# Optimization experiments

Measured on AMD Instinct MI355X. Metric: run time of the kernel, lower is better.

Reference implementation:

```python
import jax, jax.numpy as jnp
import numpy as np

B, IMG, P, C_IN, D, NH, DEPTH, E, TOPK, NCLS = 8, 224, 16, 3, 768, 12, 12, 8, 2, 1000
DH = 4 * D
HD = D // NH
GRID = IMG // P
NPAT = GRID * GRID
MOE_POS = (1, 3, 5, 7, 9, 11)
N_DENSE = DEPTH - len(MOE_POS)
N_MOE = len(MOE_POS)


def setup_inputs() -> dict:
    key = jax.random.key(0)
    ks = iter(jax.random.split(key, 32))
    n = lambda shape: jax.random.normal(next(ks), shape, jnp.float32) * 0.02
    return dict(
        x=jax.random.normal(next(ks), (B, C_IN, IMG, IMG), jnp.float32),
        patch_w=n((D, C_IN * P * P)), patch_b=jnp.zeros((D,), jnp.float32),
        cls_token=n((1, 1, D)), pos_embed=n((1, NPAT + 1, D)),
        ln1_w=jnp.ones((DEPTH, D), jnp.float32), ln1_b=jnp.zeros((DEPTH, D), jnp.float32),
        qkv_w=n((DEPTH, 3 * D, D)), qkv_b=jnp.zeros((DEPTH, 3 * D), jnp.float32),
        proj_w=n((DEPTH, D, D)), proj_b=jnp.zeros((DEPTH, D), jnp.float32),
        ln2_w=jnp.ones((DEPTH, D), jnp.float32), ln2_b=jnp.zeros((DEPTH, D), jnp.float32),
        fc1_w=n((N_DENSE, DH, D)), fc1_b=jnp.zeros((N_DENSE, DH), jnp.float32),
        fc2_w=n((N_DENSE, D, DH)), fc2_b=jnp.zeros((N_DENSE, D), jnp.float32),
        gate_w=n((N_MOE, E, D)), gate_b=jnp.zeros((N_MOE, E), jnp.float32),
        exp_w1=n((N_MOE, E, DH, D)), exp_b1=jnp.zeros((N_MOE, E, DH), jnp.float32),
        exp_w2=n((N_MOE, E, D, DH)), exp_b2=jnp.zeros((N_MOE, E, D), jnp.float32),
        norm_w=jnp.ones((D,), jnp.float32), norm_b=jnp.zeros((D,), jnp.float32),
        head_w=n((NCLS, D)), head_b=jnp.zeros((NCLS,), jnp.float32),
    )


def _ln(x, w, b):
    m = x.mean(-1, keepdims=True)
    v = ((x - m) ** 2).mean(-1, keepdims=True)
    return (x - m) / jnp.sqrt(v + 1e-5) * w + b


def _attn(x, qw, qb, pw, pb):
    Bn, N, _ = x.shape
    qkv = (x @ qw.T + qb).reshape(Bn, N, 3, NH, HD).transpose(2, 0, 3, 1, 4)
    q, k, v = qkv[0], qkv[1], qkv[2]  # [B, NH, N, HD]
    a = jax.nn.softmax(jnp.einsum('bhnd,bhmd->bhnm', q, k) * HD ** -0.5, -1)
    o = jnp.einsum('bhnm,bhmd->bhnd', a, v).transpose(0, 2, 1, 3).reshape(Bn, N, D)
    return o @ pw.T + pb


def _moe(x, gw, gb, w1, b1, w2, b2):
    # FMoETransformerMLP with NaiveGate: top-2 routing, softmax over top-k logits.
    shp = x.shape
    xf = x.reshape(-1, D)  # [T, D]
    logits = xf @ gw.T + gb  # [T, E]
    vals, idx = jax.lax.top_k(logits, TOPK)
    sc = jax.nn.softmax(vals, -1)  # [T, TOPK]
    comb = (jax.nn.one_hot(idx, E, dtype=xf.dtype) * sc[..., None]).sum(1)  # [T, E]
    h = jax.nn.gelu(jnp.einsum('td,ehd->teh', xf, w1) + b1, approximate=False)
    y = jnp.einsum('teh,edh->ted', h, w2) + b2
    return (y * comb[..., None]).sum(1).reshape(shp)


def reference(x, patch_w, patch_b, cls_token, pos_embed, ln1_w, ln1_b, qkv_w, qkv_b, proj_w, proj_b, ln2_w, ln2_b, fc1_w, fc1_b, fc2_w, fc2_b, gate_w, gate_b, exp_w1, exp_b1, exp_w2, exp_b2, norm_w, norm_b, head_w, head_b):
    patches = x.reshape(B, C_IN, GRID, P, GRID, P).transpose(0, 2, 4, 1, 3, 5).reshape(B, NPAT, C_IN * P * P)
    z = jnp.concatenate([jnp.broadcast_to(cls_token, (B, 1, D)), patches @ patch_w.T + patch_b], 1) + pos_embed
    di = mi = 0
    for i in range(DEPTH):
        z = z + _attn(_ln(z, ln1_w[i], ln1_b[i]), qkv_w[i], qkv_b[i], proj_w[i], proj_b[i])
        h2 = _ln(z, ln2_w[i], ln2_b[i])
        if i in MOE_POS:
            z = z + _moe(h2, gate_w[mi], gate_b[mi], exp_w1[mi], exp_b1[mi], exp_w2[mi], exp_b2[mi])
            mi += 1
        else:
            z = z + (jax.nn.gelu(h2 @ fc1_w[di].T + fc1_b[di], approximate=False) @ fc2_w[di].T + fc2_b[di])
            di += 1
    z = _ln(z, norm_w, norm_b)
    return z[:, 0] @ head_w.T + head_b
```

## Files before the change

kernel.cpp:

```cpp
#include <hip/hip_runtime.h>
#include <hip/hip_bf16.h>
#include <math.h>

#define B_     8
#define IMG_   224
#define PATCH_ 16
#define CIN_   3
#define D_     768
#define NH_    12
#define DEPTH_ 12
#define NE_    8
#define NCLS_  1000
#define DH_    3072
#define HD_    64
#define GRD_   14
#define NPAT_  196
#define NTOK_  197
#define T_     (B_*NTOK_)
#define TP_    (B_*NPAT_)
#define NSLOT_ (T_*2)

typedef __bf16 bf16_t;
typedef __bf16 bf16x8 __attribute__((ext_vector_type(8)));
typedef __bf16 bf16x4 __attribute__((ext_vector_type(4)));
typedef float  f32x4  __attribute__((ext_vector_type(4)));

static __device__ __forceinline__ float gelu_f(float x){
    return 0.5f * x * (1.0f + erff(x * 0.70710678118654752440f));
}

__global__ __launch_bounds__(256) void k_cvt(const float* __restrict__ in,
                                             bf16_t* __restrict__ out, int n){
    int i = (blockIdx.x*256 + threadIdx.x)*8;
    if (i >= n) return;
    float4 a = *reinterpret_cast<const float4*>(in + i);
    float4 b = *reinterpret_cast<const float4*>(in + i + 4);
    bf16x8 h;
    h[0]=(bf16_t)a.x; h[1]=(bf16_t)a.y; h[2]=(bf16_t)a.z; h[3]=(bf16_t)a.w;
    h[4]=(bf16_t)b.x; h[5]=(bf16_t)b.y; h[6]=(bf16_t)b.z; h[7]=(bf16_t)b.w;
    *reinterpret_cast<bf16x8*>(out + i) = h;
}

__global__ void k_patch_gather(const float* __restrict__ x, bf16_t* __restrict__ pbuf){
    int idx = blockIdx.x*256 + threadIdx.x;
    if (idx >= TP_*D_) return;
    int k  = idx % D_;
    int tp = idx / D_;
    int p  = tp % NPAT_, b = tp / NPAT_;
    int c  = k >> 8;
    int ij = k & 255;
    int i  = ij >> 4, j = ij & 15;
    int gi = p / GRD_, gj = p % GRD_;
    pbuf[idx] = (bf16_t)x[(((size_t)b*CIN_ + c)*IMG_ + gi*PATCH_ + i)*IMG_ + gj*PATCH_ + j];
}

template<int ACT, int GATHER, int MOE, int OUTBF, int KSPLIT, int PARTIAL, int BMT, int NW>
__global__ __launch_bounds__(NW*64) void k_mgemm(
    const bf16_t* __restrict__ A, const int* __restrict__ gidx,
    const bf16_t* __restrict__ W, const float* __restrict__ bias,
    void* __restrict__ Cout, int M, int N, int K,
    const int* __restrict__ moff, const int* __restrict__ mcnt)
{
    __shared__ __align__(16) bf16_t As[BMT*64];
    __shared__ __align__(16) bf16_t Bs[128*64];
    const int tid = threadIdx.x, lane = tid & 63, w = tid >> 6;
    int row_begin, Mhi, ksid;
    if (MOE) {
        const int e = blockIdx.z;
        const int o = moff[e], c = mcnt[e];
        const int rb = (KSPLIT == 2) ? (int)(blockIdx.y >> 1) : (int)blockIdx.y;
        ksid = (KSPLIT == 2) ? (int)(blockIdx.y & 1) : 0;
        row_begin = o + rb*BMT;
        Mhi = o + c;
        if (row_begin >= Mhi) return;
        W += (size_t)e*N*K;
        if (!PARTIAL) bias += (size_t)e*N;
    } else {
        row_begin = blockIdx.y*BMT;
        ksid = (KSPLIT == 2) ? (int)blockIdx.z : 0;
        Mhi = M;
    }
    const int bn = blockIdx.x*128;
    const int KL = K / KSPLIT;

    const bf16_t* aG[2];
    int aOff[2];
    #pragma unroll
    for (int i = 0; i < 2; ++i) {
        const int s = w*2 + i;
        const int row_l = s*8 + (lane >> 3);
        const int cc = (lane & 7) ^ (row_l & 7);
        const int gg = min(row_begin + row_l, Mhi - 1);
        const int tok = GATHER ? (gidx[gg] >> 1) : gg;
        aG[i] = A + (size_t)tok*K + ksid*KL + cc*8;
        aOff[i] = s*512;
    }
    constexpr int NB = 16/NW;
    const bf16_t* wG[NB];
    int wOff[NB];
    #pragma unroll
    for (int j = 0; j < NB; ++j) {
        const int s = w*NB + j;
        const int row_l = s*8 + (lane >> 3);
        const int cc = (lane & 7) ^ (row_l & 7);
        wG[j] = W + (size_t)(bn + row_l)*K + ksid*KL + cc*8;
        wOff[j] = s*512;
    }
    const int wm = (w >> 1)*32, wn = (w & 1)*64;
    const int fr = lane & 15, kg = lane >> 4;
    int offA[2][2], offB[2][4];
    #pragma unroll
    for (int ks = 0; ks < 2; ++ks) {
        #pragma unroll
        for (int t = 0; t < 2; ++t) {
            const int ra = wm + t*16 + fr;
            offA[ks][t] = ra*128 + (((ks*4 + kg) ^ (ra & 7)) << 4);
        }
        #pragma unroll
        for (int t = 0; t < 4; ++t) {
            const int rb2 = wn + t*16 + fr;
            offB[ks][t] = rb2*128 + (((ks*4 + kg) ^ (rb2 & 7)) << 4);
        }
    }

    f32x4 acc[2][4] = {};
    const int nt = KL >> 6;
    for (int t = 0; t < nt; ++t) {
        if (t) __syncthreads();
        #pragma unroll
        for (int i = 0; i < 2; ++i) {
            __builtin_amdgcn_global_load_lds(
                (const __attribute__((address_space(1))) void*)(aG[i]),
                (__attribute__((address_space(3))) void*)(&As[aOff[i]]), 16, 0, 0);
            aG[i] += 64;
        }
        #pragma unroll
        for (int j = 0; j < NB; ++j) {
            __builtin_amdgcn_global_load_lds(
                (const __attribute__((address_space(1))) void*)(wG[j]),
                (__attribute__((address_space(3))) void*)(&Bs[wOff[j]]), 16, 0, 0);
            wG[j] += 64;
        }
        __syncthreads();
        const char* baseA = (const char*)&As[0];
        const char* baseB = (const char*)&Bs[0];
        #pragma unroll
        for (int ks = 0; ks < 2; ++ks) {
            bf16x8 af[2], bf[4];
            #pragma unroll
            for (int t2 = 0; t2 < 2; ++t2)
                af[t2] = *reinterpret_cast<const bf16x8*>(baseA + offA[ks][t2]);
            #pragma unroll
            for (int t2 = 0; t2 < 4; ++t2)
                bf[t2] = *reinterpret_cast<const bf16x8*>(baseB + offB[ks][t2]);
            #pragma unroll
            for (int mt = 0; mt < 2; ++mt)
                #pragma unroll
                for (int nt2 = 0; nt2 < 4; ++nt2)
                    acc[mt][nt2] = __builtin_amdgcn_mfma_f32_16x16x32_bf16(
                        af[mt], bf[nt2], acc[mt][nt2], 0, 0, 0);
        }
    }
    float*  Cf = (float*)Cout + ((PARTIAL && KSPLIT == 2) ? (size_t)ksid*M*N : (size_t)0);
    bf16_t* Cb = (bf16_t*)Cout;
    const int cr = kg*4;
    #pragma unroll
    for (int nt2 = 0; nt2 < 4; ++nt2) {
        const int n = bn + wn + nt2*16 + fr;
        const float bv = PARTIAL ? 0.0f : bias[n];
        #pragma unroll
        for (int mt = 0; mt < 2; ++mt) {
            #pragma unroll
            for (int r2 = 0; r2 < 4; ++r2) {
                const int m = row_begin + wm + mt*16 + cr + r2;
                if (m < Mhi) {
                    float v = acc[mt][nt2][r2] + bv;
                    if (ACT) v = gelu_f(v);
                    if (OUTBF) Cb[(size_t)m*N + n] = (bf16_t)v;
                    else       Cf[(size_t)m*N + n] = v;
                }
            }
        }
    }
}

struct LNOut { float y0, y1, y2; };
static __device__ __forceinline__ LNOut ln_block(float v0, float v1, float v2,
        const float* __restrict__ w, const float* __restrict__ b,
        float* red, int tid)
{
    const int wid = tid >> 6, lane = tid & 63;
    float s = v0 + v1 + v2;
    for (int m=32;m>0;m>>=1) s += __shfl_xor(s, m);
    if (lane == 0) red[wid] = s;
    __syncthreads();
    if (tid == 0) red[4] = (red[0]+red[1]+red[2]+red[3]) * (1.0f/768.0f);
    __syncthreads();
    const float mean = red[4];
    float d0 = v0-mean, d1 = v1-mean, d2 = v2-mean;
    float q = d0*d0 + d1*d1 + d2*d2;
    for (int m=32;m>0;m>>=1) q += __shfl_xor(q, m);
    if (lane == 0) red[wid] = q;
    __syncthreads();
    if (tid == 0) {
        float var = (red[0]+red[1]+red[2]+red[3]) * (1.0f/768.0f);
        red[5] = 1.0f / sqrtf(var + 1e-5f);
    }
    __syncthreads();
    const float rstd = red[5];
    LNOut o;
    o.y0 = d0*rstd*w[tid    ] + b[tid    ];
    o.y1 = d1*rstd*w[tid+256] + b[tid+256];
    o.y2 = d2*rstd*w[tid+512] + b[tid+512];
    return o;
}

template<typename TOUT>
__global__ __launch_bounds__(256) void k_ln(const float* __restrict__ X,
        const float* __restrict__ w, const float* __restrict__ b,
        TOUT* __restrict__ Y, int in_mul)
{
    __shared__ float red[8];
    const int r = blockIdx.x, tid = threadIdx.x;
    const float* xr = X + (size_t)r*in_mul*D_;
    LNOut o = ln_block(xr[tid], xr[tid+256], xr[tid+512], w, b, red, tid);
    TOUT* yr = Y + (size_t)r*D_;
    yr[tid] = (TOUT)o.y0; yr[tid+256] = (TOUT)o.y1; yr[tid+512] = (TOUT)o.y2;
}

__global__ __launch_bounds__(256) void k_asmln(const float* __restrict__ pe,
        const float* __restrict__ cls, const float* __restrict__ pos,
        float* __restrict__ z, const float* __restrict__ w,
        const float* __restrict__ b, bf16_t* __restrict__ Y)
{
    __shared__ float red[8];
    const int t = blockIdx.x, tid = threadIdx.x;
    const int bb = t / NTOK_, r = t % NTOK_;
    float v[3];
    #pragma unroll
    for (int j = 0; j < 3; ++j) {
        const int n = tid + j*256;
        if (r == 0) v[j] = cls[n] + pos[n];
        else        v[j] = pe[((size_t)bb*NPAT_ + (r-1))*D_ + n] + pos[(size_t)r*D_ + n];
        z[(size_t)t*D_ + n] = v[j];
    }
    LNOut o = ln_block(v[0], v[1], v[2], w, b, red, tid);
    bf16_t* yr = Y + (size_t)t*D_;
    yr[tid] = (bf16_t)o.y0; yr[tid+256] = (bf16_t)o.y1; yr[tid+512] = (bf16_t)o.y2;
}

template<int GATE, int NP>
__global__ __launch_bounds__(256) void k_addln(
    float* __restrict__ z, const float* __restrict__ P,
    const float* __restrict__ bias,
    const float* __restrict__ w, const float* __restrict__ b,
    bf16_t* __restrict__ Y,
    const float* __restrict__ gw, const float* __restrict__ gb,
    int* __restrict__ t_e, float* __restrict__ t_sc)
{
    __shared__ float red[8];
    __shared__ float red2[4][8];
    const int t = blockIdx.x, tid = threadIdx.x;
    const int wid = tid >> 6, lane = tid & 63;
    const float* P1 = P + (size_t)T_*D_;
    float v[3];
    #pragma unroll
    for (int j = 0; j < 3; ++j) {
        const int n = tid + j*256;
        float nv = z[(size_t)t*D_+n] + P[(size_t)t*D_+n] + bias[n];
        if (NP == 2) nv += P1[(size_t)t*D_+n];
        z[(size_t)t*D_+n] = nv;
        v[j] = nv;
    }
    LNOut o = ln_block(v[0], v[1], v[2], w, b, red, tid);
    bf16_t* yr = Y + (size_t)t*D_;
    yr[tid] = (bf16_t)o.y0; yr[tid+256] = (bf16_t)o.y1; yr[tid+512] = (bf16_t)o.y2;
    if (GATE) {
        float p[NE_];
        #pragma unroll
        for (int e = 0; e < NE_; ++e)
            p[e] = o.y0*gw[e*D_+tid] + o.y1*gw[e*D_+tid+256] + o.y2*gw[e*D_+tid+512];
        #pragma unroll
        for (int e = 0; e < NE_; ++e)
            for (int m=32;m>0;m>>=1) p[e] += __shfl_xor(p[e], m);
        if (lane == 0)
            #pragma unroll
            for (int e = 0; e < NE_; ++e) red2[wid][e] = p[e];
        __syncthreads();
        if (tid == 0) {
            float l[NE_];
            #pragma unroll
            for (int e = 0; e < NE_; ++e)
                l[e] = red2[0][e]+red2[1][e]+red2[2][e]+red2[3][e] + gb[e];
            int i0 = 0;
            for (int e = 1; e < NE_; ++e) if (l[e] > l[i0]) i0 = e;
            int i1 = -1;
            for (int e = 0; e < NE_; ++e) if (e != i0 && (i1 < 0 || l[e] > l[i1])) i1 = e;
            float e1 = __expf(l[i1] - l[i0]);
            float s = 1.0f + e1;
            t_e[t*2]   = i0;   t_e[t*2+1]  = i1;
            t_sc[t*2]  = 1.0f/s; t_sc[t*2+1] = e1/s;
        }
    }
}

__global__ __launch_bounds__(1024) void k_scansc(const int* __restrict__ t_e,
        int* __restrict__ gidx, int* __restrict__ rg,
        int* __restrict__ offs, int* __restrict__ counts)
{
    __shared__ int h[NE_], o[NE_], c2[NE_];
    const int tid = threadIdx.x;
    if (tid < NE_) h[tid] = 0;
    __syncthreads();
    for (int id = tid; id < NSLOT_; id += 1024) atomicAdd(&h[t_e[id]], 1);
    __syncthreads();
    if (tid == 0) {
        int s = 0;
        for (int e = 0; e < NE_; ++e) { o[e] = s; s += h[e]; c2[e] = 0; }
    }
    __syncthreads();
    if (tid < NE_) { offs[tid] = o[tid]; counts[tid] = h[tid]; }
    for (int id = tid; id < NSLOT_; id += 1024) {
        int e = t_e[id];
        int pos = atomicAdd(&c2[e], 1);
        int g = o[e] + pos;
        gidx[g] = id;
        rg[id] = g;
    }
}

template<int LN>
__global__ __launch_bounds__(256) void k_comb(
    const float* __restrict__ mp, const float* __restrict__ b2,
    const int* __restrict__ t_e, const int* __restrict__ rg,
    const float* __restrict__ t_sc, float* __restrict__ z,
    const float* __restrict__ w, const float* __restrict__ b,
    bf16_t* __restrict__ Y)
{
    __shared__ float red[8];
    const int t = blockIdx.x, tid = threadIdx.x;
    const int g0 = rg[2*t], g1 = rg[2*t+1];
    const int e0 = t_e[2*t], e1 = t_e[2*t+1];
    const float s0 = t_sc[2*t], s1 = t_sc[2*t+1];
    const float* mp1 = mp + (size_t)NSLOT_*D_;
    float v[3];
    #pragma unroll
    for (int j = 0; j < 3; ++j) {
        const int n = tid + j*256;
        float y0 = mp[(size_t)g0*D_+n] + mp1[(size_t)g0*D_+n] + b2[(size_t)e0*D_+n];
        float y1 = mp[(size_t)g1*D_+n] + mp1[(size_t)g1*D_+n] + b2[(size_t)e1*D_+n];
        float nv = z[(size_t)t*D_+n] + s0*y0 + s1*y1;
        z[(size_t)t*D_+n] = nv;
        v[j] = nv;
    }
    if (LN) {
        LNOut o = ln_block(v[0], v[1], v[2], w, b, red, tid);
        bf16_t* yr = Y + (size_t)t*D_;
        yr[tid] = (bf16_t)o.y0; yr[tid+256] = (bf16_t)o.y1; yr[tid+512] = (bf16_t)o.y2;
    }
}

__global__ __launch_bounds__(256) void k_attn(const bf16_t* __restrict__ qkv,
                                              bf16_t* __restrict__ out)
{
    __shared__ bf16_t Kl[NTOK_*68];
    __shared__ float  qs[8][64];
    __shared__ bf16_t ps[8][200];
    const int qb = blockIdx.x*8;
    const int h = blockIdx.y, b = blockIdx.z;
    const int tid = threadIdx.x, lane = tid & 63, wid = tid >> 6;
    for (int id = tid; id < NTOK_*8; id += 256) {
        const int m = id >> 3, c = id & 7;
        bf16x8 v = *reinterpret_cast<const bf16x8*>(
            qkv + (size_t)(b*NTOK_+m)*2304 + 768 + h*HD_ + c*8);
        bf16x4 lo = {v[0],v[1],v[2],v[3]}, hi = {v[4],v[5],v[6],v[7]};
        *reinterpret_cast<bf16x4*>(&Kl[m*68 + c*8    ]) = lo;
        *reinterpret_cast<bf16x4*>(&Kl[m*68 + c*8 + 4]) = hi;
    }
    for (int id = tid; id < 512; id += 256) {
        const int qq = id >> 6, d = id & 63;
        const int n = qb + qq;
        qs[qq][d] = (n < NTOK_) ? (float)qkv[(size_t)(b*NTOK_+n)*2304 + h*HD_ + d] : 0.0f;
    }
    __syncthreads();
    const int na = qb + wid, nb = qb + wid + 4;
    const bool va = na < NTOK_, vb = nb < NTOK_;
    if (!va) return;
    float sa[4] = {0,0,0,0}, sb[4] = {0,0,0,0};
    for (int d = 0; d < HD_; d += 4) {
        const f32x4 qa = *reinterpret_cast<const f32x4*>(&qs[wid][d]);
        const f32x4 qv = *reinterpret_cast<const f32x4*>(&qs[wid+4][d]);
        #pragma unroll
        for (int j = 0; j < 4; ++j) {
            const int m = lane + 64*j;
            const int mc = m < NTOK_ ? m : NTOK_-1;
            bf16x4 kv = *reinterpret_cast<const bf16x4*>(&Kl[mc*68 + d]);
            float k0=(float)kv[0], k1=(float)kv[1], k2=(float)kv[2], k3=(float)kv[3];
            sa[j] += qa[0]*k0 + qa[1]*k1 + qa[2]*k2 + qa[3]*k3;
            sb[j] += qv[0]*k0 + qv[1]*k1 + qv[2]*k2 + qv[3]*k3;
        }
    }
    #pragma unroll
    for (int j = 0; j < 4; ++j) {
        const bool ok = (lane + 64*j) < NTOK_;
        sa[j] = ok ? sa[j]*0.125f : -3.0e38f;
        sb[j] = ok ? sb[j]*0.125f : -3.0e38f;
    }
    float mxa = fmaxf(fmaxf(sa[0],sa[1]), fmaxf(sa[2],sa[3]));
    float mxb = fmaxf(fmaxf(sb[0],sb[1]), fmaxf(sb[2],sb[3]));
    for (int m=32;m>0;m>>=1) { mxa = fmaxf(mxa, __shfl_xor(mxa,m)); mxb = fmaxf(mxb, __shfl_xor(mxb,m)); }
    float pa[4], pb[4], suma = 0.0f, sumb = 0.0f;
    #pragma unroll
    for (int j = 0; j < 4; ++j) {
        pa[j] = __expf(sa[j]-mxa); suma += pa[j];
        pb[j] = __expf(sb[j]-mxb); sumb += pb[j];
    }
    for (int m=32;m>0;m>>=1) { suma += __shfl_xor(suma,m); sumb += __shfl_xor(sumb,m); }
    #pragma unroll
    for (int j = 0; j < 4; ++j) {
        const int m = lane + 64*j;
        if (m < NTOK_) {
            ps[wid][m] = (bf16_t)pa[j];
            if (vb) ps[wid+4][m] = (bf16_t)pb[j];
        }
    }
    const float inva = 1.0f/suma, invb = 1.0f/sumb;
    const bf16_t* vbase = qkv + (size_t)b*NTOK_*2304 + 1536 + h*HD_ + lane;
    float aa = 0.0f, ab = 0.0f;
    if (vb) {
        for (int m = 0; m < NTOK_; ++m) {
            const float vv = (float)vbase[(size_t)m*2304];
            aa += (float)ps[wid][m]*vv;
            ab += (float)ps[wid+4][m]*vv;
        }
    } else {
        for (int m = 0; m < NTOK_; ++m)
            aa += (float)ps[wid][m]*(float)vbase[(size_t)m*2304];
    }
    out[(size_t)(b*NTOK_+na)*D_ + h*HD_ + lane] = (bf16_t)(aa*inva);
    if (vb) out[(size_t)(b*NTOK_+nb)*D_ + h*HD_ + lane] = (bf16_t)(ab*invb);
}

__global__ __launch_bounds__(256) void k_head(const float* __restrict__ zn,
        const float* __restrict__ hw, const float* __restrict__ hb,
        float* __restrict__ out)
{
    const int o = blockIdx.x*4 + (threadIdx.x >> 6);
    const int b = blockIdx.y;
    const int lane = threadIdx.x & 63;
    if (o >= NCLS_) return;
    float acc = 0.0f;
    #pragma unroll 4
    for (int k = lane; k < D_; k += 64)
        acc = fmaf(zn[b*D_+k], hw[(size_t)o*D_+k], acc);
    for (int m=32;m>0;m>>=1) acc += __shfl_xor(acc, m);
    if (lane == 0) out[b*NCLS_+o] = acc + hb[o];
}

extern "C" void kernel_launch(void* const* d_in, const int* in_sizes, int n_in,
                              void* d_out, int out_size, void* d_ws, size_t ws_size,
                              hipStream_t stream)
{
    const float* x        = (const float*)d_in[0];
    const float* patch_w  = (const float*)d_in[1];
    const float* patch_b  = (const float*)d_in[2];
    const float* cls_tok  = (const float*)d_in[3];
    const float* pos_emb  = (const float*)d_in[4];
    const float* ln1_w    = (const float*)d_in[5];
    const float* ln1_b    = (const float*)d_in[6];
    const float* qkv_w    = (const float*)d_in[7];
    const float* qkv_b    = (const float*)d_in[8];
    const float* proj_w   = (const float*)d_in[9];
    const float* proj_b   = (const float*)d_in[10];
    const float* ln2_w    = (const float*)d_in[11];
    const float* ln2_b    = (const float*)d_in[12];
    const float* fc1_w    = (const float*)d_in[13];
    const float* fc1_b    = (const float*)d_in[14];
    const float* fc2_w    = (const float*)d_in[15];
    const float* fc2_b    = (const float*)d_in[16];
    const float* gate_w   = (const float*)d_in[17];
    const float* gate_b   = (const float*)d_in[18];
    const float* exp_w1   = (const float*)d_in[19];
    const float* exp_b1   = (const float*)d_in[20];
    const float* exp_w2   = (const float*)d_in[21];
    const float* exp_b2   = (const float*)d_in[22];
    const float* norm_w   = (const float*)d_in[23];
    const float* norm_b   = (const float*)d_in[24];
    const float* head_w   = (const float*)d_in[25];
    const float* head_b   = (const float*)d_in[26];

    char* wsb = (char*)d_ws;
    size_t off_ = 0;
    auto alloc = [&](size_t nelem, size_t esz) -> void* {
        void* p = wsb + off_;
        off_ += ((nelem*esz + 255) / 256) * 256;
        return p;
    };
    float*  z      = (float*) alloc((size_t)T_*D_, 4);
    bf16_t* lnbuf  = (bf16_t*)alloc((size_t)T_*D_, 2);
    bf16_t* qkvbuf = (bf16_t*)alloc((size_t)T_*3*D_, 2);
    bf16_t* abuf   = (bf16_t*)alloc((size_t)T_*D_, 2);
    bf16_t* hid    = (bf16_t*)alloc((size_t)NSLOT_*DH_, 2);
    float*  pp     = (float*) alloc((size_t)2*T_*D_, 4);
    float*  mp     = (float*) alloc((size_t)2*NSLOT_*D_, 4);
    float*  t_sc   = (float*) alloc(NSLOT_, 4);
    float*  zn     = (float*) alloc((size_t)B_*D_, 4);
    int*    t_e    = (int*)   alloc(NSLOT_, 4);
    int*    rg     = (int*)   alloc(NSLOT_, 4);
    int*    gidx   = (int*)   alloc(NSLOT_, 4);
    int*    offs   = (int*)   alloc(8, 4);
    int*    counts = (int*)   alloc(8, 4);
    const size_t n_patch = (size_t)D_*D_;
    const size_t n_qkv   = (size_t)DEPTH_*3*D_*D_;
    const size_t n_proj  = (size_t)DEPTH_*D_*D_;
    const size_t n_fc1   = (size_t)6*DH_*D_;
    const size_t n_fc2   = (size_t)6*D_*DH_;
    const size_t n_e1    = (size_t)6*NE_*DH_*D_;
    const size_t n_e2    = (size_t)6*NE_*D_*DH_;
    bf16_t* wb_patch = (bf16_t*)alloc(n_patch, 2);
    bf16_t* wb_qkv   = (bf16_t*)alloc(n_qkv, 2);
    bf16_t* wb_proj  = (bf16_t*)alloc(n_proj, 2);
    bf16_t* wb_fc1   = (bf16_t*)alloc(n_fc1, 2);
    bf16_t* wb_fc2   = (bf16_t*)alloc(n_fc2, 2);
    bf16_t* wb_e1    = (bf16_t*)alloc(n_e1, 2);
    bf16_t* wb_e2    = (bf16_t*)alloc(n_e2, 2);
    bf16_t* pbuf   = hid;
    float*  pout   = mp;

    auto cvt = [&](const float* src, bf16_t* dst, size_t n){
        k_cvt<<<dim3((unsigned)((n/8 + 255)/256)), 256, 0, stream>>>(src, dst, (int)n);
    };
    cvt(patch_w, wb_patch, n_patch);
    cvt(qkv_w,   wb_qkv,   n_qkv);
    cvt(proj_w,  wb_proj,  n_proj);
    cvt(fc1_w,   wb_fc1,   n_fc1);
    cvt(fc2_w,   wb_fc2,   n_fc2);
    cvt(exp_w1,  wb_e1,    n_e1);
    cvt(exp_w2,  wb_e2,    n_e2);

    k_patch_gather<<<dim3((TP_*D_+255)/256), 256, 0, stream>>>(x, pbuf);
    k_mgemm<0,0,0,0,1,0,64,4><<<dim3(D_/128, (TP_+63)/64), 256, 0, stream>>>(
        pbuf, nullptr, wb_patch, patch_b, pout, TP_, D_, D_, nullptr, nullptr);
    k_asmln<<<T_, 256, 0, stream>>>(pout, cls_tok, pos_emb, z, ln1_w, ln1_b, lnbuf);

    const int GY64  = (T_+63)/64;
    const int GY128 = (T_+127)/128;
    int di = 0, mi = 0;
    for (int i = 0; i < DEPTH_; ++i){
        k_mgemm<0,0,0,1,1,0,64,4><<<dim3(3*D_/128, GY64), 256, 0, stream>>>(
            lnbuf, nullptr, wb_qkv + (size_t)i*3*D_*D_, qkv_b + (size_t)i*3*D_,
            qkvbuf, T_, 3*D_, D_, nullptr, nullptr);
        k_attn<<<dim3((NTOK_+7)/8, NH_, B_), 256, 0, stream>>>(qkvbuf, abuf);
        k_mgemm<0,0,0,0,1,1,64,4><<<dim3(D_/128, GY64), 256, 0, stream>>>(
            abuf, nullptr, wb_proj + (size_t)i*D_*D_, nullptr,
            pp, T_, D_, D_, nullptr, nullptr);
        if (i & 1){
            k_addln<1,1><<<T_, 256, 0, stream>>>(z, pp, proj_b + i*D_,
                ln2_w + i*D_, ln2_b + i*D_, lnbuf,
                gate_w + (size_t)mi*NE_*D_, gate_b + (size_t)mi*NE_, t_e, t_sc);
            k_scansc<<<1, 1024, 0, stream>>>(t_e, gidx, rg, offs, counts);
            k_mgemm<1,1,1,1,1,0,128,8><<<dim3(DH_/128, 25, NE_), 512, 0, stream>>>(
                lnbuf, gidx, wb_e1 + (size_t)mi*NE_*DH_*D_, exp_b1 + (size_t)mi*NE_*DH_,
                hid, NSLOT_, DH_, D_, offs, counts);
            k_mgemm<0,0,1,0,2,1,128,8><<<dim3(D_/128, 50, NE_), 512, 0, stream>>>(
                hid, nullptr, wb_e2 + (size_t)mi*NE_*D_*DH_, nullptr,
                mp, NSLOT_, D_, DH_, offs, counts);
            if (i + 1 < DEPTH_) {
                k_comb<1><<<T_, 256, 0, stream>>>(mp, exp_b2 + (size_t)mi*NE_*D_,
                    t_e, rg, t_sc, z, ln1_w + (i+1)*D_, ln1_b + (i+1)*D_, lnbuf);
            } else {
                k_comb<0><<<T_, 256, 0, stream>>>(mp, exp_b2 + (size_t)mi*NE_*D_,
                    t_e, rg, t_sc, z, nullptr, nullptr, nullptr);
            }
            mi++;
        } else {
            k_addln<0,1><<<T_, 256, 0, stream>>>(z, pp, proj_b + i*D_,
                ln2_w + i*D_, ln2_b + i*D_, lnbuf,
                nullptr, nullptr, nullptr, nullptr);
            k_mgemm<1,0,0,1,1,0,128,8><<<dim3(DH_/128, GY128), 512, 0, stream>>>(
                lnbuf, nullptr, wb_fc1 + (size_t)di*DH_*D_, fc1_b + (size_t)di*DH_,
                hid, T_, DH_, D_, nullptr, nullptr);
            k_mgemm<0,0,0,0,2,1,64,4><<<dim3(D_/128, GY64, 2), 256, 0, stream>>>(
                hid, nullptr, wb_fc2 + (size_t)di*D_*DH_, nullptr,
                pp, T_, D_, DH_, nullptr, nullptr);
            k_addln<0,2><<<T_, 256, 0, stream>>>(z, pp, fc2_b + di*D_,
                ln1_w + (i+1)*D_, ln1_b + (i+1)*D_, lnbuf,
                nullptr, nullptr, nullptr, nullptr);
            di++;
        }
    }
    k_ln<float><<<B_, 256, 0, stream>>>(z, norm_w, norm_b, zn, NTOK_);
    k_head<<<dim3((NCLS_+3)/4, B_), 256, 0, stream>>>(zn, head_w, head_b, (float*)d_out);
}
```

Measured before the change: 2.659 ms.

## Double-buffer LDS tiles in GEMM to overlap global loads with MFMA

The GEMM kernel now keeps two LDS buffers for the A and B tiles and issues the next K-tile's global-to-LDS loads before computing on the current tile. Explicit vmcnt waits and s_barrier calls stand in for the old syncthreads pair. The aim is to hide global memory latency behind MFMA work. In exchange LDS use doubles, which may reduce occupancy, and the hand-set vmcnt counts must match the number of loads issued per tile.

```diff
diff --git a/kernel.cpp b/kernel.cpp
--- a/kernel.cpp
+++ b/kernel.cpp
@@ -61,8 +61,8 @@
     void* __restrict__ Cout, int M, int N, int K,
     const int* __restrict__ moff, const int* __restrict__ mcnt)
 {
-    __shared__ __align__(16) bf16_t As[BMT*64];
-    __shared__ __align__(16) bf16_t Bs[128*64];
+    __shared__ __align__(16) bf16_t As[2][BMT*64];
+    __shared__ __align__(16) bf16_t Bs[2][128*64];
     const int tid = threadIdx.x, lane = tid & 63, w = tid >> 6;
     int row_begin, Mhi, ksid;
     if (MOE) {
@@ -123,27 +123,39 @@
         }
     }
 
-    f32x4 acc[2][4] = {};
-    const int nt = KL >> 6;
-    for (int t = 0; t < nt; ++t) {
-        if (t) __syncthreads();
+    auto issue = [&](int sb) {
         #pragma unroll
         for (int i = 0; i < 2; ++i) {
             __builtin_amdgcn_global_load_lds(
                 (const __attribute__((address_space(1))) void*)(aG[i]),
-                (__attribute__((address_space(3))) void*)(&As[aOff[i]]), 16, 0, 0);
+                (__attribute__((address_space(3))) void*)(&As[sb][aOff[i]]), 16, 0, 0);
             aG[i] += 64;
         }
         #pragma unroll
         for (int j = 0; j < NB; ++j) {
             __builtin_amdgcn_global_load_lds(
                 (const __attribute__((address_space(1))) void*)(wG[j]),
-                (__attribute__((address_space(3))) void*)(&Bs[wOff[j]]), 16, 0, 0);
+                (__attribute__((address_space(3))) void*)(&Bs[sb][wOff[j]]), 16, 0, 0);
             wG[j] += 64;
         }
-        __syncthreads();
-        const char* baseA = (const char*)&As[0];
-        const char* baseB = (const char*)&Bs[0];
+    };
+
+    f32x4 acc[2][4] = {};
+    const int nt = KL >> 6;
+    issue(0);
+    for (int t = 0; t < nt; ++t) {
+        if (t + 1 < nt) {
+            issue((t + 1) & 1);
+            if constexpr (NW == 4) asm volatile("s_waitcnt vmcnt(6)" ::: "memory");
+            else                   asm volatile("s_waitcnt vmcnt(4)" ::: "memory");
+        } else {
+            asm volatile("s_waitcnt vmcnt(0)" ::: "memory");
+        }
+        __builtin_amdgcn_sched_barrier(0);
+        __builtin_amdgcn_s_barrier();
+        __builtin_amdgcn_sched_barrier(0);
+        const char* baseA = (const char*)&As[t & 1][0];
+        const char* baseB = (const char*)&Bs[t & 1][0];
         #pragma unroll
         for (int ks = 0; ks < 2; ++ks) {
             bf16x8 af[2], bf[4];
@@ -159,6 +171,11 @@
                 for (int nt2 = 0; nt2 < 4; ++nt2)
                     acc[mt][nt2] = __builtin_amdgcn_mfma_f32_16x16x32_bf16(
                         af[mt], bf[nt2], acc[mt][nt2], 0, 0, 0);
+        }
+        if (t + 1 < nt) {
+            __builtin_amdgcn_sched_barrier(0);
+            __builtin_amdgcn_s_barrier();
+            __builtin_amdgcn_sched_barrier(0);
         }
     }
     float*  Cf = (float*)Cout + ((PARTIAL && KSPLIT == 2) ? (size_t)ksid*M*N : (size_t)0);
```

New measurement: 2.673 ms. No clear change (+0.5%).

## Add 4-stage global_load_lds ring GEMM for dense layers and fuse weight conversion

Applied to the files above, without the earlier changes.

Adds a new 128x128-tile GEMM kernel that streams A and W tiles straight into LDS through global_load_lds. It keeps a four-buffer ring with vmcnt-based waits, so memory loads overlap with MFMA compute. The patch, QKV, proj, fc1 and fc2 GEMMs now use it instead of the older mgemm. The seven weight-conversion launches become a single kernel, and the attention PV loop gets an unroll pragma. The larger tiles reduce grid size for T=1576, which may lower occupancy and parallelism; the kernel uses 128KB of LDS per block.

```diff
diff --git a/kernel.cpp b/kernel.cpp
--- a/kernel.cpp
+++ b/kernel.cpp
@@ -29,16 +29,40 @@
     return 0.5f * x * (1.0f + erff(x * 0.70710678118654752440f));
 }
 
-__global__ __launch_bounds__(256) void k_cvt(const float* __restrict__ in,
-                                             bf16_t* __restrict__ out, int n){
-    int i = (blockIdx.x*256 + threadIdx.x)*8;
-    if (i >= n) return;
-    float4 a = *reinterpret_cast<const float4*>(in + i);
-    float4 b = *reinterpret_cast<const float4*>(in + i + 4);
+__global__ __launch_bounds__(256) void k_cvt_all(
+    const float* __restrict__ s0, bf16_t* __restrict__ d0,
+    const float* __restrict__ s1, bf16_t* __restrict__ d1,
+    const float* __restrict__ s2, bf16_t* __restrict__ d2,
+    const float* __restrict__ s3, bf16_t* __restrict__ d3,
+    const float* __restrict__ s4, bf16_t* __restrict__ d4,
+    const float* __restrict__ s5, bf16_t* __restrict__ d5,
+    const float* __restrict__ s6, bf16_t* __restrict__ d6)
+{
+    constexpr size_t n0 = (size_t)D_*D_;
+    constexpr size_t n1 = (size_t)DEPTH_*3*D_*D_;
+    constexpr size_t n2 = (size_t)DEPTH_*D_*D_;
+    constexpr size_t n3 = (size_t)6*DH_*D_;
+    constexpr size_t n4 = (size_t)6*D_*DH_;
+    constexpr size_t n5 = (size_t)6*NE_*DH_*D_;
+    constexpr size_t n6 = (size_t)6*NE_*D_*DH_;
+    constexpr size_t c0 = n0, c1 = c0+n1, c2 = c1+n2, c3 = c2+n3,
+                     c4 = c3+n4, c5 = c4+n5, c6 = c5+n6;
+    size_t i = ((size_t)blockIdx.x*256 + threadIdx.x)*8;
+    if (i >= c6) return;
+    const float* src; bf16_t* dst; size_t off;
+    if      (i < c0) { src = s0; dst = d0; off = i; }
+    else if (i < c1) { src = s1; dst = d1; off = i - c0; }
+    else if (i < c2) { src = s2; dst = d2; off = i - c1; }
+    else if (i < c3) { src = s3; dst = d3; off = i - c2; }
+    else if (i < c4) { src = s4; dst = d4; off = i - c3; }
+    else if (i < c5) { src = s5; dst = d5; off = i - c4; }
+    else             { src = s6; dst = d6; off = i - c5; }
+    float4 a = *reinterpret_cast<const float4*>(src + off);
+    float4 b = *reinterpret_cast<const float4*>(src + off + 4);
     bf16x8 h;
     h[0]=(bf16_t)a.x; h[1]=(bf16_t)a.y; h[2]=(bf16_t)a.z; h[3]=(bf16_t)a.w;
     h[4]=(bf16_t)b.x; h[5]=(bf16_t)b.y; h[6]=(bf16_t)b.z; h[7]=(bf16_t)b.w;
-    *reinterpret_cast<bf16x8*>(out + i) = h;
+    *reinterpret_cast<bf16x8*>(dst + off) = h;
 }
 
 __global__ void k_patch_gather(const float* __restrict__ x, bf16_t* __restrict__ pbuf){
@@ -184,6 +208,116 @@
     }
 }
 
+template<int ACT, int OUTBF, int KSPLIT, int PARTIAL>
+__global__ __launch_bounds__(256) void k_mgemm_ring(
+    const bf16_t* __restrict__ A,
+    const bf16_t* __restrict__ W, const float* __restrict__ bias,
+    void* __restrict__ Cout, int M, int N, int K)
+{
+    __shared__ __align__(16) bf16_t As[4][128*64];
+    __shared__ __align__(16) bf16_t Bs[4][128*64];
+    const int tid = threadIdx.x, lane = tid & 63, w = tid >> 6;
+    const int wr = w >> 1, wc = w & 1;
+    const int row_begin = blockIdx.y*128;
+    const int ksid = (KSPLIT == 2) ? (int)blockIdx.z : 0;
+    const int Mhi = M;
+    const int bn = blockIdx.x*128;
+    const int KL = K / KSPLIT;
+
+    const bf16_t* aG[4];
+    const bf16_t* wG[4];
+    int sOff[4];
+    #pragma unroll
+    for (int i = 0; i < 4; ++i) {
+        const int s = w*4 + i;
+        const int row_l = s*8 + (lane >> 3);
+        const int cc = (lane & 7) ^ (row_l & 7);
+        const int gg = min(row_begin + row_l, Mhi - 1);
+        aG[i] = A + (size_t)gg*K + ksid*KL + cc*8;
+        wG[i] = W + (size_t)(bn + row_l)*K + ksid*KL + cc*8;
+        sOff[i] = s*512;
+    }
+    const int fr = lane & 15, kg = lane >> 4;
+    int offA[2][4], offB[2][4];
+    #pragma unroll
+    for (int ks = 0; ks < 2; ++ks)
+        #pragma unroll
+        for (int t = 0; t < 4; ++t) {
+            const int ra = wr*64 + t*16 + fr;
+            const int rb2 = wc*64 + t*16 + fr;
+            offA[ks][t] = ra*128 + (((ks*4 + kg) ^ (ra & 7)) << 4);
+            offB[ks][t] = rb2*128 + (((ks*4 + kg) ^ (rb2 & 7)) << 4);
+        }
+
+    auto issue = [&](int sb) {
+        #pragma unroll
+        for (int i = 0; i < 4; ++i) {
+            __builtin_amdgcn_global_load_lds(
+                (const __attribute__((address_space(1))) void*)(aG[i]),
+                (__attribute__((address_space(3))) void*)(&As[sb][sOff[i]]), 16, 0, 0);
+            aG[i] += 64;
+            __builtin_amdgcn_global_load_lds(
+                (const __attribute__((address_space(1))) void*)(wG[i]),
+                (__attribute__((address_space(3))) void*)(&Bs[sb][sOff[i]]), 16, 0, 0);
+            wG[i] += 64;
+        }
+    };
+
+    f32x4 acc[4][4] = {};
+    const int nt = KL >> 6;
+    issue(0);
+    if (nt > 1) issue(1);
+    if (nt > 2) issue(2);
+    for (int t = 0; t < nt; ++t) {
+        const int rem = nt - 1 - t;
+        if (rem >= 2)      asm volatile("s_waitcnt vmcnt(16)" ::: "memory");
+        else if (rem == 1) asm volatile("s_waitcnt vmcnt(8)" ::: "memory");
+        else               asm volatile("s_waitcnt vmcnt(0)" ::: "memory");
+        __builtin_amdgcn_sched_barrier(0);
+        __builtin_amdgcn_s_barrier();
+        __builtin_amdgcn_sched_barrier(0);
+        if (t + 3 < nt) issue((t + 3) & 3);
+        const char* baseA = (const char*)&As[t & 3][0];
+        const char* baseB = (const char*)&Bs[t & 3][0];
+        #pragma unroll
+        for (int ks = 0; ks < 2; ++ks) {
+            bf16x8 af[4], bf[4];
+            #pragma unroll
+            for (int t2 = 0; t2 < 4; ++t2) {
+                af[t2] = *reinterpret_cast<const bf16x8*>(baseA + offA[ks][t2]);
+                bf[t2] = *reinterpret_cast<const bf16x8*>(baseB + offB[ks][t2]);
+            }
+            #pragma unroll
+            for (int mt = 0; mt < 4; ++mt)
+                #pragma unroll
+                for (int nt2 = 0; nt2 < 4; ++nt2)
+                    acc[mt][nt2] = __builtin_amdgcn_mfma_f32_16x16x32_bf16(
+                        af[mt], bf[nt2], acc[mt][nt2], 0, 0, 0);
+        }
+    }
+    float*  Cf = (float*)Cout + ((PARTIAL && KSPLIT == 2) ? (size_t)ksid*M*N : (size_t)0);
+    bf16_t* Cb = (bf16_t*)Cout;
+    const int cr = kg*4;
+    #pragma unroll
+    for (int nt2 = 0; nt2 < 4; ++nt2) {
+        const int n = bn + wc*64 + nt2*16 + fr;
+        const float bv = PARTIAL ? 0.0f : bias[n];
+        #pragma unroll
+        for (int mt = 0; mt < 4; ++mt) {
+            #pragma unroll
+            for (int r2 = 0; r2 < 4; ++r2) {
+                const int m = row_begin + wr*64 + mt*16 + cr + r2;
+                if (m < Mhi) {
+                    float v = acc[mt][nt2][r2] + bv;
+                    if (ACT) v = gelu_f(v);
+                    if (OUTBF) Cb[(size_t)m*N + n] = (bf16_t)v;
+                    else       Cf[(size_t)m*N + n] = v;
+                }
+            }
+        }
+    }
+}
+
 struct LNOut { float y0, y1, y2; };
 static __device__ __forceinline__ LNOut ln_block(float v0, float v1, float v2,
         const float* __restrict__ w, const float* __restrict__ b,
@@ -428,12 +562,14 @@
     const bf16_t* vbase = qkv + (size_t)b*NTOK_*2304 + 1536 + h*HD_ + lane;
     float aa = 0.0f, ab = 0.0f;
     if (vb) {
+        #pragma unroll 4
         for (int m = 0; m < NTOK_; ++m) {
             const float vv = (float)vbase[(size_t)m*2304];
             aa += (float)ps[wid][m]*vv;
             ab += (float)ps[wid+4][m]*vv;
         }
     } else {
+        #pragma unroll 4
         for (int m = 0; m < NTOK_; ++m)
             aa += (float)ps[wid][m]*(float)vbase[(size_t)m*2304];
     }
@@ -527,33 +663,26 @@
     bf16_t* pbuf   = hid;
     float*  pout   = mp;
 
-    auto cvt = [&](const float* src, bf16_t* dst, size_t n){
-        k_cvt<<<dim3((unsigned)((n/8 + 255)/256)), 256, 0, stream>>>(src, dst, (int)n);
-    };
-    cvt(patch_w, wb_patch, n_patch);
-    cvt(qkv_w,   wb_qkv,   n_qkv);
-    cvt(proj_w,  wb_proj,  n_proj);
-    cvt(fc1_w,   wb_fc1,   n_fc1);
-    cvt(fc2_w,   wb_fc2,   n_fc2);
-    cvt(exp_w1,  wb_e1,    n_e1);
-    cvt(exp_w2,  wb_e2,    n_e2);
+    const size_t total = n_patch+n_qkv+n_proj+n_fc1+n_fc2+n_e1+n_e2;
+    k_cvt_all<<<dim3((unsigned)((total/8 + 255)/256)), 256, 0, stream>>>(
+        patch_w, wb_patch, qkv_w, wb_qkv, proj_w, wb_proj,
+        fc1_w, wb_fc1, fc2_w, wb_fc2, exp_w1, wb_e1, exp_w2, wb_e2);
 
     k_patch_gather<<<dim3((TP_*D_+255)/256), 256, 0, stream>>>(x, pbuf);
-    k_mgemm<0,0,0,0,1,0,64,4><<<dim3(D_/128, (TP_+63)/64), 256, 0, stream>>>(
-        pbuf, nullptr, wb_patch, patch_b, pout, TP_, D_, D_, nullptr, nullptr);
+    k_mgemm_ring<0,0,1,0><<<dim3(D_/128, (TP_+127)/128), 256, 0, stream>>>(
+        pbuf, wb_patch, patch_b, pout, TP_, D_, D_);
     k_asmln<<<T_, 256, 0, stream>>>(pout, cls_tok, pos_emb, z, ln1_w, ln1_b, lnbuf);
 
-    const int GY64  = (T_+63)/64;
     const int GY128 = (T_+127)/128;
     int di = 0, mi = 0;
     for (int i = 0; i < DEPTH_; ++i){
-        k_mgemm<0,0,0,1,1,0,64,4><<<dim3(3*D_/128, GY64), 256, 0, stream>>>(
-            lnbuf, nullptr, wb_qkv + (size_t)i*3*D_*D_, qkv_b + (size_t)i*3*D_,
-            qkvbuf, T_, 3*D_, D_, nullptr, nullptr);
+        k_mgemm_ring<0,1,1,0><<<dim3(3*D_/128, GY128), 256, 0, stream>>>(
+            lnbuf, wb_qkv + (size_t)i*3*D_*D_, qkv_b + (size_t)i*3*D_,
+            qkvbuf, T_, 3*D_, D_);
         k_attn<<<dim3((NTOK_+7)/8, NH_, B_), 256, 0, stream>>>(qkvbuf, abuf);
-        k_mgemm<0,0,0,0,1,1,64,4><<<dim3(D_/128, GY64), 256, 0, stream>>>(
-            abuf, nullptr, wb_proj + (size_t)i*D_*D_, nullptr,
-            pp, T_, D_, D_, nullptr, nullptr);
+        k_mgemm_ring<0,0,1,1><<<dim3(D_/128, GY128), 256, 0, stream>>>(
+            abuf, wb_proj + (size_t)i*D_*D_, nullptr,
+            pp, T_, D_, D_);
         if (i & 1){
             k_addln<1,1><<<T_, 256, 0, stream>>>(z, pp, proj_b + i*D_,
                 ln2_w + i*D_, ln2_b + i*D_, lnbuf,
@@ -577,12 +706,12 @@
             k_addln<0,1><<<T_, 256, 0, stream>>>(z, pp, proj_b + i*D_,
                 ln2_w + i*D_, ln2_b + i*D_, lnbuf,
                 nullptr, nullptr, nullptr, nullptr);
-            k_mgemm<1,0,0,1,1,0,128,8><<<dim3(DH_/128, GY128), 512, 0, stream>>>(
-                lnbuf, nullptr, wb_fc1 + (size_t)di*DH_*D_, fc1_b + (size_t)di*DH_,
-                hid, T_, DH_, D_, nullptr, nullptr);
-            k_mgemm<0,0,0,0,2,1,64,4><<<dim3(D_/128, GY64, 2), 256, 0, stream>>>(
-                hid, nullptr, wb_fc2 + (size_t)di*D_*DH_, nullptr,
-                pp, T_, D_, DH_, nullptr, nullptr);
+            k_mgemm_ring<1,1,1,0><<<dim3(DH_/128, GY128), 256, 0, stream>>>(
+                lnbuf, wb_fc1 + (size_t)di*DH_*D_, fc1_b + (size_t)di*DH_,
+                hid, T_, DH_, D_);
+            k_mgemm_ring<0,0,2,1><<<dim3(D_/128, GY128, 2), 256, 0, stream>>>(
+                hid, wb_fc2 + (size_t)di*D_*DH_, nullptr,
+                pp, T_, D_, DH_);
             k_addln<0,2><<<T_, 256, 0, stream>>>(z, pp, fc2_b + di*D_,
                 ln1_w + (i+1)*D_, ln1_b + (i+1)*D_, lnbuf,
                 nullptr, nullptr, nullptr, nullptr);
```

Result: slower. 3.362 ms (+26.5%).
